# Performance work log

Hardware: AMD Instinct MI355X
Metric: run time of the kernel (lower is better)

## Reference

```python
import jax, jax.numpy as jnp
import numpy as np

NUM_USER, NUM_ITEM, NUM_TAG, K = 100000, 1000000, 100000, 64
B = 1048576


def setup_inputs() -> dict:
    key = jax.random.key(0)
    ks = jax.random.split(key, 8)
    lim = np.sqrt(3.0 / K).astype(np.float32)
    return {
        "x": jax.random.randint(ks[0], (B, 4), 0, NUM_USER, dtype=jnp.int64) if jax.config.jax_enable_x64 else jax.random.randint(ks[0], (B, 4), 0, NUM_USER, dtype=jnp.int32),
        "user_vecs": jax.random.normal(ks[1], (NUM_USER, K), dtype=jnp.float32) * 0.01,
        "item_vecs": jax.random.normal(ks[2], (NUM_ITEM, K), dtype=jnp.float32) * 0.01,
        "tag_vecs": jax.random.normal(ks[3], (NUM_TAG, K), dtype=jnp.float32) * 0.01,
        "w_user": jax.random.uniform(ks[4], (K, K), jnp.float32, -lim, lim),
        "b_user": jnp.zeros((K,), jnp.float32),
        "w_item": jax.random.uniform(ks[5], (K, K), jnp.float32, -lim, lim),
        "b_item": jnp.zeros((K,), jnp.float32),
    }


def reference(x, user_vecs, item_vecs, tag_vecs, w_user, b_user, w_item, b_item):
    # gathers: [B, K]
    user_vec = user_vecs[x[:, 0]]
    item_vec = item_vecs[x[:, 1]]
    tag_vec = tag_vecs[x[:, 2]]
    neg_tag_vec = tag_vecs[x[:, 3]]
    # nn.Linear: y = t @ W.T + b, then sigmoid
    ut = jax.nn.sigmoid(tag_vec @ w_user.T + b_user)
    it = jax.nn.sigmoid(tag_vec @ w_item.T + b_item)
    nut = jax.nn.sigmoid(neg_tag_vec @ w_user.T + b_user)
    nit = jax.nn.sigmoid(neg_tag_vec @ w_item.T + b_item)
    r = (jnp.sum(user_vec * ut, axis=1) + jnp.sum(item_vec * it, axis=1)
         - (jnp.sum(user_vec * nut, axis=1) + jnp.sum(item_vec * nit, axis=1)))
    return r
```

## Files before the change

kernel.cpp:

```cpp
#include <hip/hip_runtime.h>


__device__ __forceinline__ float sigmoidf_(float z) {
    return 1.0f / (1.0f + __expf(-z));
}

__global__ __launch_bounds__(256) void precompute_tags(
    const float* __restrict__ tag_vecs,
    const float* __restrict__ w_user, const float* __restrict__ b_user,
    const float* __restrict__ w_item, const float* __restrict__ b_item,
    float* __restrict__ UT, float* __restrict__ IT, int num_tag)
{
    __shared__ float wu[64 * 64];
    __shared__ float wi[64 * 64];
    __shared__ float bu[64];
    __shared__ float bi[64];

    for (int i = threadIdx.x; i < 1024; i += 256) {
        ((float4*)wu)[i] = ((const float4*)w_user)[i];
        ((float4*)wi)[i] = ((const float4*)w_item)[i];
    }
    if (threadIdx.x < 64) {
        bu[threadIdx.x] = b_user[threadIdx.x];
        bi[threadIdx.x] = b_item[threadIdx.x];
    }
    __syncthreads();

    int tag = blockIdx.x * 256 + threadIdx.x;
    if (tag >= num_tag) return;

    float4 tv[16];
    const float4* tp = (const float4*)(tag_vecs + (size_t)tag * 64);
    #pragma unroll
    for (int k = 0; k < 16; ++k) tv[k] = tp[k];

    float4* utp = (float4*)(UT + (size_t)tag * 64);
    float4* itp = (float4*)(IT + (size_t)tag * 64);

    #pragma unroll 4
    for (int j4 = 0; j4 < 16; ++j4) {
        float4 zu, zi;
        float* zup = (float*)&zu;
        float* zip = (float*)&zi;
        #pragma unroll
        for (int jj = 0; jj < 4; ++jj) {
            int j = j4 * 4 + jj;
            float au = bu[j];
            float ai = bi[j];
            const float4* wur = (const float4*)(wu + j * 64);
            const float4* wir = (const float4*)(wi + j * 64);
            #pragma unroll
            for (int k = 0; k < 16; ++k) {
                float4 a = wur[k];
                float4 b = wir[k];
                float4 t = tv[k];
                au += t.x * a.x + t.y * a.y + t.z * a.z + t.w * a.w;
                ai += t.x * b.x + t.y * b.y + t.z * b.z + t.w * b.w;
            }
            zup[jj] = sigmoidf_(au);
            zip[jj] = sigmoidf_(ai);
        }
        utp[j4] = zu;
        itp[j4] = zi;
    }
}

__global__ __launch_bounds__(256) void score_kernel(
    const int* __restrict__ x,
    const float* __restrict__ user_vecs,
    const float* __restrict__ item_vecs,
    const float* __restrict__ UT, const float* __restrict__ IT,
    float* __restrict__ out, int B)
{
    int sub = threadIdx.x & 15;
    int row0 = (blockIdx.x * 256 + threadIdx.x) >> 4;
    int rstride = (gridDim.x * 256) >> 4;

    for (int row = row0; row < B; row += rstride) {
        int4 idx = ((const int4*)x)[row];

        const float4* up   = (const float4*)(user_vecs + (size_t)idx.x * 64);
        const float4* ip   = (const float4*)(item_vecs + (size_t)idx.y * 64);
        const float4* utp  = (const float4*)(UT + (size_t)idx.z * 64);
        const float4* itp  = (const float4*)(IT + (size_t)idx.z * 64);
        const float4* nutp = (const float4*)(UT + (size_t)idx.w * 64);
        const float4* nitp = (const float4*)(IT + (size_t)idx.w * 64);

        float4 u  = up[sub];
        float4 iv = ip[sub];
        float4 a  = utp[sub];
        float4 b  = nutp[sub];
        float4 c  = itp[sub];
        float4 d  = nitp[sub];

        float p = u.x * (a.x - b.x) + u.y * (a.y - b.y)
                + u.z * (a.z - b.z) + u.w * (a.w - b.w)
                + iv.x * (c.x - d.x) + iv.y * (c.y - d.y)
                + iv.z * (c.z - d.z) + iv.w * (c.w - d.w);

        p += __shfl_xor(p, 1);
        p += __shfl_xor(p, 2);
        p += __shfl_xor(p, 4);
        p += __shfl_xor(p, 8);

        if (sub == 0) out[row] = p;
    }
}

__global__ __launch_bounds__(256) void fused_fallback(
    const int* __restrict__ x,
    const float* __restrict__ user_vecs,
    const float* __restrict__ item_vecs,
    const float* __restrict__ tag_vecs,
    const float* __restrict__ w_user, const float* __restrict__ b_user,
    const float* __restrict__ w_item, const float* __restrict__ b_item,
    float* __restrict__ out, int B)
{
    int tid = blockIdx.x * 256 + threadIdx.x;
    int row = tid >> 6;
    int lane = tid & 63;
    if (row >= B) return;

    int4 idx = ((const int4*)x)[row];

    float t  = tag_vecs[(size_t)idx.z * 64 + lane];
    float nt = tag_vecs[(size_t)idx.w * 64 + lane];

    const float* wur = w_user + lane * 64;
    const float* wir = w_item + lane * 64;

    float zu = b_user[lane], zi = b_item[lane];
    float nzu = zu, nzi = zi;
    #pragma unroll 8
    for (int k = 0; k < 64; ++k) {
        float tk  = __shfl(t, k, 64);
        float ntk = __shfl(nt, k, 64);
        float wuk = wur[k];
        float wik = wir[k];
        zu  += tk * wuk;  zi  += tk * wik;
        nzu += ntk * wuk; nzi += ntk * wik;
    }

    float ut  = sigmoidf_(zu);
    float itg = sigmoidf_(zi);
    float nut = sigmoidf_(nzu);
    float nit = sigmoidf_(nzi);

    float uv = user_vecs[(size_t)idx.x * 64 + lane];
    float ivv = item_vecs[(size_t)idx.y * 64 + lane];
    float p = uv * (ut - nut) + ivv * (itg - nit);

    #pragma unroll
    for (int off = 32; off; off >>= 1) p += __shfl_xor(p, off, 64);

    if (lane == 0) out[row] = p;
}

extern "C" void kernel_launch(void* const* d_in, const int* in_sizes, int n_in,
                              void* d_out, int out_size, void* d_ws, size_t ws_size,
                              hipStream_t stream) {
    const int*   x         = (const int*)d_in[0];
    const float* user_vecs = (const float*)d_in[1];
    const float* item_vecs = (const float*)d_in[2];
    const float* tag_vecs  = (const float*)d_in[3];
    const float* w_user    = (const float*)d_in[4];
    const float* b_user    = (const float*)d_in[5];
    const float* w_item    = (const float*)d_in[6];
    const float* b_item    = (const float*)d_in[7];
    float* out = (float*)d_out;

    const int B = in_sizes[0] / 4;
    const int num_tag = in_sizes[3] / 64;
    const size_t need = 2ull * (size_t)num_tag * 64 * sizeof(float);

    if (ws_size >= need) {
        float* UT = (float*)d_ws;
        float* IT = UT + (size_t)num_tag * 64;
        precompute_tags<<<(num_tag + 255) / 256, 256, 0, stream>>>(
            tag_vecs, w_user, b_user, w_item, b_item, UT, IT, num_tag);
        int nblocks = (B * 16 + 255) / 256;
        if (nblocks > 65536) nblocks = 65536;
        score_kernel<<<nblocks, 256, 0, stream>>>(
            x, user_vecs, item_vecs, UT, IT, out, B);
    } else {
        fused_fallback<<<((size_t)B * 64 + 255) / 256, 256, 0, stream>>>(
            x, user_vecs, item_vecs, tag_vecs,
            w_user, b_user, w_item, b_item, out, B);
    }
}
```

Measured before the change: 596.5 us.

## Store precomputed tag sigmoids as interleaved fp16 offsets in one table

The precomputed per-tag user and item sigmoid tables are now stored as fp16 with 0.5 subtracted, to improve precision near zero. The two tables are interleaved into one 256-byte row per tag, so the score kernel fetches one 16-byte chunk per tag instead of two separate float4 loads. This halves the gathered bytes for tag data and halves the table's footprint, which helps it stay in cache, at the cost of fp16 rounding error. The constant offset cancels in the positive-minus-negative difference. The output store is also made nontemporal.

```diff
diff --git a/kernel.cpp b/kernel.cpp
--- a/kernel.cpp
+++ b/kernel.cpp
@@ -1,15 +1,23 @@
 #include <hip/hip_runtime.h>
+#include <hip/hip_fp16.h>
 
 
 __device__ __forceinline__ float sigmoidf_(float z) {
     return 1.0f / (1.0f + __expf(-z));
+}
+
+__device__ __forceinline__ int h2_as_int(__half2 h) {
+    union { __half2 h; int i; } u; u.h = h; return u.i;
+}
+__device__ __forceinline__ __half2 int_as_h2(int i) {
+    union { __half2 h; int i; } u; u.i = i; return u.h;
 }
 
 __global__ __launch_bounds__(256) void precompute_tags(
     const float* __restrict__ tag_vecs,
     const float* __restrict__ w_user, const float* __restrict__ b_user,
     const float* __restrict__ w_item, const float* __restrict__ b_item,
-    float* __restrict__ UT, float* __restrict__ IT, int num_tag)
+    int4* __restrict__ C, int num_tag)
 {
     __shared__ float wu[64 * 64];
     __shared__ float wi[64 * 64];
@@ -34,17 +42,16 @@
     #pragma unroll
     for (int k = 0; k < 16; ++k) tv[k] = tp[k];
 
-    float4* utp = (float4*)(UT + (size_t)tag * 64);
-    float4* itp = (float4*)(IT + (size_t)tag * 64);
-
-    #pragma unroll 4
-    for (int j4 = 0; j4 < 16; ++j4) {
-        float4 zu, zi;
-        float* zup = (float*)&zu;
-        float* zip = (float*)&zi;
+    int4* crow = C + (size_t)tag * 16;
+
+    #pragma unroll 2
+    for (int c = 0; c < 16; ++c) {
+        float d0, d1, d2, d3, e0, e1, e2, e3;
+        float* dd[4] = {&d0, &d1, &d2, &d3};
+        float* ee[4] = {&e0, &e1, &e2, &e3};
         #pragma unroll
         for (int jj = 0; jj < 4; ++jj) {
-            int j = j4 * 4 + jj;
+            int j = 4 * c + jj;
             float au = bu[j];
             float ai = bi[j];
             const float4* wur = (const float4*)(wu + j * 64);
@@ -57,11 +64,15 @@
                 au += t.x * a.x + t.y * a.y + t.z * a.z + t.w * a.w;
                 ai += t.x * b.x + t.y * b.y + t.z * b.z + t.w * b.w;
             }
-            zup[jj] = sigmoidf_(au);
-            zip[jj] = sigmoidf_(ai);
+            *dd[jj] = sigmoidf_(au) - 0.5f;
+            *ee[jj] = sigmoidf_(ai) - 0.5f;
         }
-        utp[j4] = zu;
-        itp[j4] = zi;
+        int4 pack;
+        pack.x = h2_as_int(__floats2half2_rn(d0, d1));
+        pack.y = h2_as_int(__floats2half2_rn(d2, d3));
+        pack.z = h2_as_int(__floats2half2_rn(e0, e1));
+        pack.w = h2_as_int(__floats2half2_rn(e2, e3));
+        crow[c] = pack;
     }
 }
 
@@ -69,7 +80,7 @@
     const int* __restrict__ x,
     const float* __restrict__ user_vecs,
     const float* __restrict__ item_vecs,
-    const float* __restrict__ UT, const float* __restrict__ IT,
+    const int4* __restrict__ C,
     float* __restrict__ out, int B)
 {
     int sub = threadIdx.x & 15;
@@ -79,31 +90,31 @@
     for (int row = row0; row < B; row += rstride) {
         int4 idx = ((const int4*)x)[row];
 
-        const float4* up   = (const float4*)(user_vecs + (size_t)idx.x * 64);
-        const float4* ip   = (const float4*)(item_vecs + (size_t)idx.y * 64);
-        const float4* utp  = (const float4*)(UT + (size_t)idx.z * 64);
-        const float4* itp  = (const float4*)(IT + (size_t)idx.z * 64);
-        const float4* nutp = (const float4*)(UT + (size_t)idx.w * 64);
-        const float4* nitp = (const float4*)(IT + (size_t)idx.w * 64);
-
-        float4 u  = up[sub];
-        float4 iv = ip[sub];
-        float4 a  = utp[sub];
-        float4 b  = nutp[sub];
-        float4 c  = itp[sub];
-        float4 d  = nitp[sub];
-
-        float p = u.x * (a.x - b.x) + u.y * (a.y - b.y)
-                + u.z * (a.z - b.z) + u.w * (a.w - b.w)
-                + iv.x * (c.x - d.x) + iv.y * (c.y - d.y)
-                + iv.z * (c.z - d.z) + iv.w * (c.w - d.w);
+        float4 u  = ((const float4*)(user_vecs + (size_t)idx.x * 64))[sub];
+        float4 iv = ((const float4*)(item_vecs + (size_t)idx.y * 64))[sub];
+        int4 ct = C[(size_t)idx.z * 16 + sub];
+        int4 cn = C[(size_t)idx.w * 16 + sub];
+
+        float2 dt01 = __half22float2(int_as_h2(ct.x));
+        float2 dt23 = __half22float2(int_as_h2(ct.y));
+        float2 et01 = __half22float2(int_as_h2(ct.z));
+        float2 et23 = __half22float2(int_as_h2(ct.w));
+        float2 dn01 = __half22float2(int_as_h2(cn.x));
+        float2 dn23 = __half22float2(int_as_h2(cn.y));
+        float2 en01 = __half22float2(int_as_h2(cn.z));
+        float2 en23 = __half22float2(int_as_h2(cn.w));
+
+        float p = u.x  * (dt01.x - dn01.x) + u.y  * (dt01.y - dn01.y)
+                + u.z  * (dt23.x - dn23.x) + u.w  * (dt23.y - dn23.y)
+                + iv.x * (et01.x - en01.x) + iv.y * (et01.y - en01.y)
+                + iv.z * (et23.x - en23.x) + iv.w * (et23.y - en23.y);
 
         p += __shfl_xor(p, 1);
         p += __shfl_xor(p, 2);
         p += __shfl_xor(p, 4);
         p += __shfl_xor(p, 8);
 
-        if (sub == 0) out[row] = p;
+        if (sub == 0) __builtin_nontemporal_store(p, out + row);
     }
 }
 
@@ -146,7 +157,7 @@
     float nut = sigmoidf_(nzu);
     float nit = sigmoidf_(nzi);
 
-    float uv = user_vecs[(size_t)idx.x * 64 + lane];
+    float uv  = user_vecs[(size_t)idx.x * 64 + lane];
     float ivv = item_vecs[(size_t)idx.y * 64 + lane];
     float p = uv * (ut - nut) + ivv * (itg - nit);
 
@@ -171,17 +182,16 @@
 
     const int B = in_sizes[0] / 4;
     const int num_tag = in_sizes[3] / 64;
-    const size_t need = 2ull * (size_t)num_tag * 64 * sizeof(float);
+    const size_t need = (size_t)num_tag * 256;
 
     if (ws_size >= need) {
-        float* UT = (float*)d_ws;
-        float* IT = UT + (size_t)num_tag * 64;
+        int4* C = (int4*)d_ws;
         precompute_tags<<<(num_tag + 255) / 256, 256, 0, stream>>>(
-            tag_vecs, w_user, b_user, w_item, b_item, UT, IT, num_tag);
+            tag_vecs, w_user, b_user, w_item, b_item, C, num_tag);
         int nblocks = (B * 16 + 255) / 256;
         if (nblocks > 65536) nblocks = 65536;
         score_kernel<<<nblocks, 256, 0, stream>>>(
-            x, user_vecs, item_vecs, UT, IT, out, B);
+            x, user_vecs, item_vecs, C, out, B);
     } else {
         fused_fallback<<<((size_t)B * 64 + 255) / 256, 256, 0, stream>>>(
             x, user_vecs, item_vecs, tag_vecs,
```

Result: faster. 525.9 us (-11.8%).
